# Kernel optimization log

Hardware: AMD Instinct MI355X
Metric: run time of the kernel (lower is better)

Reference implementation:

```python
import jax, jax.numpy as jnp
import numpy as np

DIM = 1024
HEADS = 8
DIM_HEAD = 64
INNER = HEADS * DIM_HEAD  # 512
LN_EPS = 1e-5


def setup_inputs() -> dict:
    key = jax.random.key(0)
    ks = jax.random.split(key, 8)
    b, n, m = 4, 2048, 512
    x = jax.random.normal(ks[0], (b, n, DIM), dtype=jnp.float32)
    media = jax.random.normal(ks[1], (b, m, DIM), dtype=jnp.float32)
    media_mask = jax.random.randint(ks[2], (b, m), 0, 2).astype(jnp.bool_)
    media_mask = media_mask.at[:, 0].set(True)  # avoid fully-masked rows
    ln_g = jnp.ones((DIM,), jnp.float32)
    ln_b = jnp.zeros((DIM,), jnp.float32)
    s = 0.02
    Wq = jax.random.normal(ks[3], (DIM, INNER), jnp.float32) * s
    Wkv = jax.random.normal(ks[4], (DIM, 2 * INNER), jnp.float32) * s
    Wo = jax.random.normal(ks[5], (INNER, DIM), jnp.float32) * s
    return {"x": x, "media": media, "media_mask": media_mask,
            "ln_g": ln_g, "ln_b": ln_b, "Wq": Wq, "Wkv": Wkv, "Wo": Wo}


def _layernorm(x, g, b):
    mu = jnp.mean(x, axis=-1, keepdims=True)
    var = jnp.var(x, axis=-1, keepdims=True)
    return (x - mu) * jax.lax.rsqrt(var + LN_EPS) * g + b


def reference(x, media, media_mask, ln_g, ln_b, Wq, Wkv, Wo):
    scale = DIM_HEAD ** (-0.5)
    xn = _layernorm(x, ln_g, ln_b)
    q = xn @ Wq                                  # (b, n, inner)
    kv = media @ Wkv                             # (b, m, 2*inner)
    k, v = jnp.split(kv, 2, axis=-1)
    # b n (h d) -> b h n d
    def split_heads(t):
        b_, s_, _ = t.shape
        return t.reshape(b_, s_, HEADS, DIM_HEAD).transpose(0, 2, 1, 3)
    q, k, v = split_heads(q) * scale, split_heads(k), split_heads(v)
    sim = jnp.einsum('bhid,bhjd->bhij', q, k)    # (b, h, n, m)
    neg_inf = jnp.finfo(sim.dtype).min
    sim = jnp.where(media_mask[:, None, None, :], sim, neg_inf)
    attn = jax.nn.softmax(sim, axis=-1)          # stable (max-subtract) softmax
    out = jnp.einsum('bhij,bhjd->bhid', attn, v)  # (b, h, n, d)
    out = out.transpose(0, 2, 1, 3).reshape(x.shape[0], x.shape[1], INNER)
    return out @ Wo
```

## Files before the change

kernel.cpp:

```cpp
#include <hip/hip_runtime.h>
#include <hip/hip_bf16.h>

typedef unsigned short u16;
typedef __attribute__((ext_vector_type(4))) unsigned short u16x4;
typedef __attribute__((ext_vector_type(8))) unsigned short u16x8;
typedef __attribute__((ext_vector_type(8))) short bf16x8;
typedef __attribute__((ext_vector_type(4))) float f32x4;

#define AS1 __attribute__((address_space(1)))
#define AS3 __attribute__((address_space(3)))

__device__ __forceinline__ float b2f(u16 v) {
    return __uint_as_float(((unsigned)v) << 16);
}
__device__ __forceinline__ u16 f2bf(float f) {
    unsigned u = __float_as_uint(f);
    unsigned r = (u + 0x7fffu + ((u >> 16) & 1u)) >> 16;
    return (u16)r;
}

__global__ __launch_bounds__(256) void prep_all(
    const float* __restrict__ x, const float* __restrict__ media,
    const unsigned char* __restrict__ mask,
    const float* __restrict__ ln_g, const float* __restrict__ ln_b,
    const float* __restrict__ Wq, const float* __restrict__ Wkv,
    const float* __restrict__ Wo,
    u16* __restrict__ xn, u16* __restrict__ mediab,
    unsigned char* __restrict__ mask8, int* __restrict__ idx,
    int* __restrict__ cnts,
    u16* __restrict__ wqt, u16* __restrict__ wkvt, u16* __restrict__ wot) {
    __shared__ u16 T[64][72];
    __shared__ int c0s, c1s;
    const int bid = blockIdx.x, tid = threadIdx.x;

    if (bid < 2048) {
        const int lane = tid & 63;
        const int row = bid * 4 + (tid >> 6);
        const float* xr = x + (size_t)row * 1024;
        float v[16];
        float sum = 0.f, sq = 0.f;
#pragma unroll
        for (int c = 0; c < 4; ++c) {
            float4 u = ((const float4*)xr)[c * 64 + lane];
            v[c * 4 + 0] = u.x; v[c * 4 + 1] = u.y; v[c * 4 + 2] = u.z; v[c * 4 + 3] = u.w;
            sum += u.x + u.y + u.z + u.w;
            sq += u.x * u.x + u.y * u.y + u.z * u.z + u.w * u.w;
        }
#pragma unroll
        for (int o = 1; o < 64; o <<= 1) {
            sum += __shfl_xor(sum, o, 64);
            sq += __shfl_xor(sq, o, 64);
        }
        float mean = sum * (1.f / 1024.f);
        float var = sq * (1.f / 1024.f) - mean * mean;
        float rs = rsqrtf(var + 1e-5f);
        u16* yr = xn + (size_t)row * 1024;
#pragma unroll
        for (int c = 0; c < 4; ++c) {
            float4 ug = ((const float4*)ln_g)[c * 64 + lane];
            float4 ub = ((const float4*)ln_b)[c * 64 + lane];
            u16x4 o;
            o[0] = f2bf((v[c * 4 + 0] - mean) * rs * ug.x + ub.x);
            o[1] = f2bf((v[c * 4 + 1] - mean) * rs * ug.y + ub.y);
            o[2] = f2bf((v[c * 4 + 2] - mean) * rs * ug.z + ub.z);
            o[3] = f2bf((v[c * 4 + 3] - mean) * rs * ug.w + ub.w);
            *(u16x4*)(yr + c * 256 + lane * 4) = o;
        }
    } else if (bid < 3072) {
        int i = (bid - 2048) * 256 + tid;
        float4 a = ((const float4*)media)[i * 2];
        float4 b = ((const float4*)media)[i * 2 + 1];
        u16x8 o;
        o[0] = f2bf(a.x); o[1] = f2bf(a.y); o[2] = f2bf(a.z); o[3] = f2bf(a.w);
        o[4] = f2bf(b.x); o[5] = f2bf(b.y); o[6] = f2bf(b.z); o[7] = f2bf(b.w);
        ((u16x8*)mediab)[i] = o;
    } else if (bid < 3840) {
        const int t = bid - 3072;
        const int z = t >> 8, rem = t & 255;
        const float* in; u16* out; int K, N;
        if (z == 0)      { in = Wq;  out = wqt;  K = 1024; N = 512; }
        else if (z == 1) { in = Wkv; out = wkvt; K = 1024; N = 1024; }
        else             { in = Wo;  out = wot;  K = 512;  N = 1024; }
        const int k0 = (rem >> 4) * 64, n0 = (rem & 15) * 64;
        if (k0 >= K || n0 >= N) return;
#pragma unroll
        for (int p = 0; p < 4; ++p) {
            int kr = p * 16 + (tid >> 4);
            float4 u = *(const float4*)(in + (size_t)(k0 + kr) * N + n0 + (tid & 15) * 4);
            u16x4 o4;
            o4[0] = f2bf(u.x); o4[1] = f2bf(u.y); o4[2] = f2bf(u.z); o4[3] = f2bf(u.w);
            *(u16x4*)(&T[kr][(tid & 15) * 4]) = o4;
        }
        __syncthreads();
        const int n = tid >> 2, kc = (tid & 3) * 16;
#pragma unroll
        for (int hh = 0; hh < 2; ++hh) {
            u16x8 o;
#pragma unroll
            for (int i = 0; i < 8; ++i) o[i] = T[kc + hh * 8 + i][n];
            *(u16x8*)(out + (size_t)(n0 + n) * K + k0 + kc + hh * 8) = o;
        }
    } else {
        if (tid == 0) { c0s = 0; c1s = 0; }
        __syncthreads();
        int a0 = 0, a1 = 0;
        for (int i = tid; i < 2048; i += 256) {
            if (mask[i]) {
                int cl = i & 3;
                if (cl == 0) a0 = 1;
                else if (cl == 1) a1 = 1;
            }
        }
        if (a0) atomicOr(&c0s, 1);
        if (a1) atomicOr(&c1s, 1);
        __syncthreads();
        int fmt = c1s ? 1 : (c0s ? 0 : 2);
        for (int e = tid; e < 2048; e += 256) {
            unsigned char v;
            if (fmt == 1)      v = (mask[e] != 0);
            else if (fmt == 0) v = (((const int*)mask)[e] != 0);
            else               v = (((const float*)mask)[e] != 0.f);
            mask8[e] = v;
        }
        __syncthreads();
        const int wv = tid >> 6, l = tid & 63;
        int off = 0;
#pragma unroll
        for (int c = 0; c < 8; ++c) {
            int key = c * 64 + l;
            bool v = mask8[wv * 512 + key] != 0;
            unsigned long long m = __ballot(v);
            int rank = __popcll(m & ((1ull << l) - 1ull));
            if (v) idx[wv * 512 + off + rank] = key;
            off += __popcll(m);
        }
        if (l == 0) cnts[wv] = off;
        int nt = (off + 31) & ~31;
        for (int p = off + l; p < nt; p += 64) idx[wv * 512 + p] = 0;
    }
}

template <int OUTF32>
__device__ __forceinline__ void gemm_tile_g(u16* As, u16* Bs,
                                            const u16* __restrict__ A,
                                            const u16* __restrict__ Bt,
                                            void* __restrict__ Cv,
                                            int N, int K, int row0, int col0,
                                            float scale) {
    const int tid = threadIdx.x;
    const int l = tid & 63, w = tid >> 6;
    const int l15 = l & 15, l4 = l >> 4;
    const int wm = w >> 1, wn = w & 1;
    const int lr = l >> 3;
    const int cs = ((l & 7) ^ lr) * 8;

    f32x4 zero = {0.f, 0.f, 0.f, 0.f};
    f32x4 acc[4][4];
#pragma unroll
    for (int i = 0; i < 4; ++i)
#pragma unroll
        for (int j = 0; j < 4; ++j) acc[i][j] = zero;

    const int rsw = l15 & 7;

    for (int k0 = 0; k0 < K; k0 += 64) {
        __syncthreads();
#pragma unroll
        for (int i = 0; i < 4; ++i) {
            int r = w * 32 + i * 8;
            __builtin_amdgcn_global_load_lds(
                (const AS1 void*)(A + (size_t)(row0 + r + lr) * K + k0 + cs),
                (AS3 void*)(As + r * 64), 16, 0, 0);
            __builtin_amdgcn_global_load_lds(
                (const AS1 void*)(Bt + (size_t)(col0 + r + lr) * K + k0 + cs),
                (AS3 void*)(Bs + r * 64), 16, 0, 0);
        }
        __syncthreads();
#pragma unroll
        for (int h = 0; h < 2; ++h) {
            bf16x8 aF[4], bF[4];
#pragma unroll
            for (int m = 0; m < 4; ++m) {
                int s = (h * 4 + l4) ^ rsw;
                aF[m] = *(const bf16x8*)(As + (wm * 64 + m * 16 + l15) * 64 + s * 8);
                bF[m] = *(const bf16x8*)(Bs + (wn * 64 + m * 16 + l15) * 64 + s * 8);
            }
#pragma unroll
            for (int m = 0; m < 4; ++m)
#pragma unroll
                for (int n = 0; n < 4; ++n)
                    acc[m][n] = __builtin_amdgcn_mfma_f32_16x16x32_bf16(aF[m], bF[n], acc[m][n], 0, 0, 0);
        }
    }
#pragma unroll
    for (int m = 0; m < 4; ++m)
#pragma unroll
        for (int n = 0; n < 4; ++n) {
            int row = row0 + wm * 64 + m * 16 + l4 * 4;
            int col = col0 + wn * 64 + n * 16 + l15;
#pragma unroll
            for (int r = 0; r < 4; ++r) {
                float vv = acc[m][n][r] * scale;
                if (OUTF32)
                    ((float*)Cv)[(size_t)(row + r) * N + col] = vv;
                else
                    ((u16*)Cv)[(size_t)(row + r) * N + col] = f2bf(vv);
            }
        }
}

__global__ __launch_bounds__(256, 2) void qkv_gemm(const u16* __restrict__ xn,
                                                   const u16* __restrict__ wqt,
                                                   u16* __restrict__ qb,
                                                   const u16* __restrict__ mediab,
                                                   const u16* __restrict__ wkvt,
                                                   u16* __restrict__ kvb) {
    __shared__ u16 As[128 * 64];
    __shared__ u16 Bs[128 * 64];
    const int b = blockIdx.x;
    const u16 *A, *Bt; u16* C; int N, row0, col0; float sc;
    if (b < 256) { A = xn;     Bt = wqt;  C = qb;  N = 512;  row0 = (b >> 2) * 128; col0 = (b & 3) * 128; sc = 0.125f; }
    else { int t = b - 256; A = mediab; Bt = wkvt; C = kvb; N = 1024; row0 = (t >> 3) * 128; col0 = (t & 7) * 128; sc = 1.f; }
    gemm_tile_g<0>(As, Bs, A, Bt, (void*)C, N, 1024, row0, col0, sc);
}

__global__ __launch_bounds__(256, 2) void o_gemm(const u16* __restrict__ ao,
                                                 const u16* __restrict__ wot,
                                                 float* __restrict__ out) {
    __shared__ u16 As[128 * 64];
    __shared__ u16 Bs[128 * 64];
    gemm_tile_g<1>(As, Bs, ao, wot, (void*)out, 1024, 512,
                   (int)blockIdx.y * 128, (int)blockIdx.x * 128, 1.f);
}

__global__ __launch_bounds__(128) void attn_mfma(const u16* __restrict__ qb,
                                                 const u16* __restrict__ kvb,
                                                 const int* __restrict__ idx,
                                                 const int* __restrict__ cnts,
                                                 u16* __restrict__ ao) {
    __shared__ u16 Ks[32][72];
    __shared__ u16 Vt[64][40];
    __shared__ u16 Pl[2][16][40];
    __shared__ int Is[512];
    const int tid = threadIdx.x;
    const int l = tid & 63, w = tid >> 6;
    const int l15 = l & 15, l4 = l >> 4;
    const int h = blockIdx.y, bbi = blockIdx.z;
    const int n0 = blockIdx.x * 32;
    const int cnt = cnts[bbi];
    const int ntile = (cnt + 31) & ~31;
    const int* ib = idx + bbi * 512;
    for (int i = tid; i < ntile; i += 128) Is[i] = ib[i];

    const u16* qp = qb + ((size_t)(bbi * 2048 + n0 + w * 16 + l15)) * 512 + h * 64;
    const bf16x8 qf0 = *(const bf16x8*)(qp + l4 * 8);
    const bf16x8 qf1 = *(const bf16x8*)(qp + 32 + l4 * 8);

    const f32x4 zero = {0.f, 0.f, 0.f, 0.f};
    f32x4 acc[4];
#pragma unroll
    for (int dt = 0; dt < 4; ++dt) acc[dt] = zero;
    float mrun[4] = {-3.0e38f, -3.0e38f, -3.0e38f, -3.0e38f};
    float lrun[4] = {0.f, 0.f, 0.f, 0.f};

    const int kj = tid >> 3, kd = (tid & 7) * 8;
    const int vj = tid & 31, vd = (tid >> 5) * 8;
    const u16* kbase = kvb + ((size_t)bbi * 512) * 1024 + h * 64;

    for (int j0 = 0; j0 < cnt; j0 += 32) {
        __syncthreads();
#pragma unroll
        for (int p = 0; p < 2; ++p) {
            int r = kj + p * 16;
            int row = Is[j0 + r];
            u16x8 kv_ = *(const u16x8*)(kbase + (size_t)row * 1024 + kd);
            *(u16x8*)(&Ks[r][kd]) = kv_;
        }
        {
            int row = Is[j0 + vj];
#pragma unroll
            for (int p = 0; p < 2; ++p) {
                int d0 = vd + p * 32;
                u16x8 vv = *(const u16x8*)(kbase + (size_t)row * 1024 + 512 + d0);
#pragma unroll
                for (int i = 0; i < 8; ++i) Vt[d0 + i][vj] = vv[i];
            }
        }
        __syncthreads();

        f32x4 s[2];
#pragma unroll
        for (int jt = 0; jt < 2; ++jt) {
            bf16x8 kf0 = *(const bf16x8*)(&Ks[jt * 16 + l15][l4 * 8]);
            bf16x8 kf1 = *(const bf16x8*)(&Ks[jt * 16 + l15][32 + l4 * 8]);
            s[jt] = __builtin_amdgcn_mfma_f32_16x16x32_bf16(qf0, kf0, zero, 0, 0, 0);
            s[jt] = __builtin_amdgcn_mfma_f32_16x16x32_bf16(qf1, kf1, s[jt], 0, 0, 0);
        }
        const float mv0 = (j0 + l15 < cnt) ? 0.f : -3.0e38f;
        const float mv1 = (j0 + 16 + l15 < cnt) ? 0.f : -3.0e38f;

#pragma unroll
        for (int r = 0; r < 4; ++r) {
            float s0 = s[0][r] + mv0;
            float s1 = s[1][r] + mv1;
            float tmax = fmaxf(s0, s1);
#pragma unroll
            for (int o = 1; o < 16; o <<= 1) tmax = fmaxf(tmax, __shfl_xor(tmax, o, 64));
            float mn = fmaxf(mrun[r], tmax);
            float p0 = (s0 > -1.0e37f) ? __expf(s0 - mn) : 0.f;
            float p1 = (s1 > -1.0e37f) ? __expf(s1 - mn) : 0.f;
            float corr = __expf(mrun[r] - mn);
            mrun[r] = mn;
            float psum = p0 + p1;
#pragma unroll
            for (int o = 1; o < 16; o <<= 1) psum += __shfl_xor(psum, o, 64);
            lrun[r] = lrun[r] * corr + psum;
#pragma unroll
            for (int dt = 0; dt < 4; ++dt) acc[dt][r] *= corr;
            Pl[w][l4 * 4 + r][l15] = f2bf(p0);
            Pl[w][l4 * 4 + r][16 + l15] = f2bf(p1);
        }
        bf16x8 pf = *(const bf16x8*)(&Pl[w][l15][l4 * 8]);
#pragma unroll
        for (int dt = 0; dt < 4; ++dt) {
            bf16x8 vf = *(const bf16x8*)(&Vt[dt * 16 + l15][l4 * 8]);
            acc[dt] = __builtin_amdgcn_mfma_f32_16x16x32_bf16(pf, vf, acc[dt], 0, 0, 0);
        }
    }

    float inv[4];
#pragma unroll
    for (int r = 0; r < 4; ++r) inv[r] = (lrun[r] > 0.f) ? (1.f / lrun[r]) : 0.f;
    u16* op = ao + ((size_t)(bbi * 2048 + n0 + w * 16)) * 512 + h * 64;
#pragma unroll
    for (int dt = 0; dt < 4; ++dt)
#pragma unroll
        for (int r = 0; r < 4; ++r)
            op[(size_t)(l4 * 4 + r) * 512 + dt * 16 + l15] = f2bf(acc[dt][r] * inv[r]);
}

extern "C" void kernel_launch(void* const* d_in, const int* in_sizes, int n_in,
                              void* d_out, int out_size, void* d_ws, size_t ws_size,
                              hipStream_t stream) {
    const float* x = (const float*)d_in[0];
    const float* media = (const float*)d_in[1];
    const unsigned char* mask = (const unsigned char*)d_in[2];
    const float* ln_g = (const float*)d_in[3];
    const float* ln_b = (const float*)d_in[4];
    const float* Wq = (const float*)d_in[5];
    const float* Wkv = (const float*)d_in[6];
    const float* Wo = (const float*)d_in[7];
    float* out = (float*)d_out;

    char* w = (char*)d_ws;
    unsigned char* mask8 = (unsigned char*)w; w += 4096;
    int* idx = (int*)w;    w += 2048 * 4;
    int* cnts = (int*)w;   w += 256;
    u16* qb = (u16*)w;     w += (size_t)8192 * 512 * 2;
    u16* kvb = (u16*)w;    w += (size_t)2048 * 1024 * 2;
    u16* ao = (u16*)w;     w += (size_t)8192 * 512 * 2;
    u16* mediab = (u16*)w; w += (size_t)2048 * 1024 * 2;
    u16* wqt = (u16*)w;    w += (size_t)512 * 1024 * 2;
    u16* wkvt = (u16*)w;   w += (size_t)1024 * 1024 * 2;
    u16* wot = (u16*)w;    w += (size_t)1024 * 512 * 2;
    u16* xn = (u16*)d_out;

    prep_all<<<3841, 256, 0, stream>>>(x, media, mask, ln_g, ln_b, Wq, Wkv, Wo,
                                       xn, mediab, mask8, idx, cnts, wqt, wkvt, wot);
    qkv_gemm<<<384, 256, 0, stream>>>(xn, wqt, qb, mediab, wkvt, kvb);
    attn_mfma<<<dim3(64, 8, 4), 128, 0, stream>>>(qb, kvb, idx, cnts, ao);
    o_gemm<<<dim3(8, 64), 256, 0, stream>>>(ao, wot, out);
}
```

Measured before the change: 88.87 us.

## Enlarge attention tiles to 64 queries and 64 keys per block iteration

The attention kernel now runs 256 threads (4 waves) covering 64 query rows per block and steps through the compacted key list 64 keys at a time instead of 32. Each staged K/V tile is shared by more waves, and the number of barrier-separated loop iterations per block is halved. The explicit masked-element check before exp is dropped because padded scores already go to zero through the large negative bias. The cost is more shared memory per block, fewer blocks in the grid (1024 instead of 2048), and more padding work when the valid key count is not a multiple of 64.

```diff
diff --git a/kernel.cpp b/kernel.cpp
--- a/kernel.cpp
+++ b/kernel.cpp
@@ -135,7 +135,7 @@
             off += __popcll(m);
         }
         if (l == 0) cnts[wv] = off;
-        int nt = (off + 31) & ~31;
+        int nt = (off + 63) & ~63;
         for (int p = off + l; p < nt; p += 64) idx[wv * 512 + p] = 0;
     }
 }
@@ -233,24 +233,24 @@
                    (int)blockIdx.y * 128, (int)blockIdx.x * 128, 1.f);
 }
 
-__global__ __launch_bounds__(128) void attn_mfma(const u16* __restrict__ qb,
+__global__ __launch_bounds__(256) void attn_mfma(const u16* __restrict__ qb,
                                                  const u16* __restrict__ kvb,
                                                  const int* __restrict__ idx,
                                                  const int* __restrict__ cnts,
                                                  u16* __restrict__ ao) {
-    __shared__ u16 Ks[32][72];
-    __shared__ u16 Vt[64][40];
-    __shared__ u16 Pl[2][16][40];
+    __shared__ u16 Ks[64][72];
+    __shared__ u16 Vt[64][72];
+    __shared__ u16 Pl[4][16][72];
     __shared__ int Is[512];
     const int tid = threadIdx.x;
     const int l = tid & 63, w = tid >> 6;
     const int l15 = l & 15, l4 = l >> 4;
     const int h = blockIdx.y, bbi = blockIdx.z;
-    const int n0 = blockIdx.x * 32;
+    const int n0 = blockIdx.x * 64;
     const int cnt = cnts[bbi];
-    const int ntile = (cnt + 31) & ~31;
+    const int ntile = (cnt + 63) & ~63;
     const int* ib = idx + bbi * 512;
-    for (int i = tid; i < ntile; i += 128) Is[i] = ib[i];
+    for (int i = tid; i < ntile; i += 256) Is[i] = ib[i];
 
     const u16* qp = qb + ((size_t)(bbi * 2048 + n0 + w * 16 + l15)) * 512 + h * 64;
     const bf16x8 qf0 = *(const bf16x8*)(qp + l4 * 8);
@@ -264,14 +264,14 @@
     float lrun[4] = {0.f, 0.f, 0.f, 0.f};
 
     const int kj = tid >> 3, kd = (tid & 7) * 8;
-    const int vj = tid & 31, vd = (tid >> 5) * 8;
+    const int vj = tid & 63, vd = (tid >> 6) * 16;
     const u16* kbase = kvb + ((size_t)bbi * 512) * 1024 + h * 64;
 
-    for (int j0 = 0; j0 < cnt; j0 += 32) {
+    for (int j0 = 0; j0 < cnt; j0 += 64) {
         __syncthreads();
 #pragma unroll
         for (int p = 0; p < 2; ++p) {
-            int r = kj + p * 16;
+            int r = kj + p * 32;
             int row = Is[j0 + r];
             u16x8 kv_ = *(const u16x8*)(kbase + (size_t)row * 1024 + kd);
             *(u16x8*)(&Ks[r][kd]) = kv_;
@@ -280,38 +280,41 @@
             int row = Is[j0 + vj];
 #pragma unroll
             for (int p = 0; p < 2; ++p) {
-                int d0 = vd + p * 32;
-                u16x8 vv = *(const u16x8*)(kbase + (size_t)row * 1024 + 512 + d0);
-#pragma unroll
-                for (int i = 0; i < 8; ++i) Vt[d0 + i][vj] = vv[i];
+                u16x8 vv = *(const u16x8*)(kbase + (size_t)row * 1024 + 512 + vd + p * 8);
+#pragma unroll
+                for (int i = 0; i < 8; ++i) Vt[vd + p * 8 + i][vj] = vv[i];
             }
         }
         __syncthreads();
 
-        f32x4 s[2];
-#pragma unroll
-        for (int jt = 0; jt < 2; ++jt) {
+        f32x4 s[4];
+        float mv[4];
+#pragma unroll
+        for (int jt = 0; jt < 4; ++jt) {
             bf16x8 kf0 = *(const bf16x8*)(&Ks[jt * 16 + l15][l4 * 8]);
             bf16x8 kf1 = *(const bf16x8*)(&Ks[jt * 16 + l15][32 + l4 * 8]);
             s[jt] = __builtin_amdgcn_mfma_f32_16x16x32_bf16(qf0, kf0, zero, 0, 0, 0);
             s[jt] = __builtin_amdgcn_mfma_f32_16x16x32_bf16(qf1, kf1, s[jt], 0, 0, 0);
-        }
-        const float mv0 = (j0 + l15 < cnt) ? 0.f : -3.0e38f;
-        const float mv1 = (j0 + 16 + l15 < cnt) ? 0.f : -3.0e38f;
+            mv[jt] = (j0 + jt * 16 + l15 < cnt) ? 0.f : -3.0e38f;
+        }
 
 #pragma unroll
         for (int r = 0; r < 4; ++r) {
-            float s0 = s[0][r] + mv0;
-            float s1 = s[1][r] + mv1;
-            float tmax = fmaxf(s0, s1);
+            float s0 = s[0][r] + mv[0];
+            float s1 = s[1][r] + mv[1];
+            float s2 = s[2][r] + mv[2];
+            float s3 = s[3][r] + mv[3];
+            float tmax = fmaxf(fmaxf(s0, s1), fmaxf(s2, s3));
 #pragma unroll
             for (int o = 1; o < 16; o <<= 1) tmax = fmaxf(tmax, __shfl_xor(tmax, o, 64));
             float mn = fmaxf(mrun[r], tmax);
-            float p0 = (s0 > -1.0e37f) ? __expf(s0 - mn) : 0.f;
-            float p1 = (s1 > -1.0e37f) ? __expf(s1 - mn) : 0.f;
+            float p0 = __expf(s0 - mn);
+            float p1 = __expf(s1 - mn);
+            float p2 = __expf(s2 - mn);
+            float p3 = __expf(s3 - mn);
             float corr = __expf(mrun[r] - mn);
             mrun[r] = mn;
-            float psum = p0 + p1;
+            float psum = (p0 + p1) + (p2 + p3);
 #pragma unroll
             for (int o = 1; o < 16; o <<= 1) psum += __shfl_xor(psum, o, 64);
             lrun[r] = lrun[r] * corr + psum;
@@ -319,12 +322,17 @@
             for (int dt = 0; dt < 4; ++dt) acc[dt][r] *= corr;
             Pl[w][l4 * 4 + r][l15] = f2bf(p0);
             Pl[w][l4 * 4 + r][16 + l15] = f2bf(p1);
-        }
-        bf16x8 pf = *(const bf16x8*)(&Pl[w][l15][l4 * 8]);
+            Pl[w][l4 * 4 + r][32 + l15] = f2bf(p2);
+            Pl[w][l4 * 4 + r][48 + l15] = f2bf(p3);
+        }
+        bf16x8 pf0 = *(const bf16x8*)(&Pl[w][l15][l4 * 8]);
+        bf16x8 pf1 = *(const bf16x8*)(&Pl[w][l15][32 + l4 * 8]);
 #pragma unroll
         for (int dt = 0; dt < 4; ++dt) {
-            bf16x8 vf = *(const bf16x8*)(&Vt[dt * 16 + l15][l4 * 8]);
-            acc[dt] = __builtin_amdgcn_mfma_f32_16x16x32_bf16(pf, vf, acc[dt], 0, 0, 0);
+            bf16x8 vf0 = *(const bf16x8*)(&Vt[dt * 16 + l15][l4 * 8]);
+            bf16x8 vf1 = *(const bf16x8*)(&Vt[dt * 16 + l15][32 + l4 * 8]);
+            acc[dt] = __builtin_amdgcn_mfma_f32_16x16x32_bf16(pf0, vf0, acc[dt], 0, 0, 0);
+            acc[dt] = __builtin_amdgcn_mfma_f32_16x16x32_bf16(pf1, vf1, acc[dt], 0, 0, 0);
         }
     }
 
@@ -368,6 +376,6 @@
     prep_all<<<3841, 256, 0, stream>>>(x, media, mask, ln_g, ln_b, Wq, Wkv, Wo,
                                        xn, mediab, mask8, idx, cnts, wqt, wkvt, wot);
     qkv_gemm<<<384, 256, 0, stream>>>(xn, wqt, qb, mediab, wkvt, kvb);
-    attn_mfma<<<dim3(64, 8, 4), 128, 0, stream>>>(qb, kvb, idx, cnts, ao);
+    attn_mfma<<<dim3(32, 8, 4), 256, 0, stream>>>(qb, kvb, idx, cnts, ao);
     o_gemm<<<dim3(8, 64), 256, 0, stream>>>(ao, wot, out);
 }
```

After: 82.50 us. 1.08x faster.
